# Optimization experiments

Hardware: AMD Instinct MI355X
Metric: run time of the kernel (lower is better)

## Reference

```python
import jax, jax.numpy as jnp
import numpy as np

DIM = 1536
HEADS = 8
DK = 64            # key_size
DV = DIM // HEADS  # value_size = 192
NPF = 32           # num_rel_pos_features
LN_EPS = 1e-3


def central_mask_features(positions, features, seq_len):
    # Borzoi/baskerville central-mask positional basis
    pow_rate = jnp.exp(jnp.log(seq_len + 1.0) / features)
    center_widths = pow_rate ** jnp.arange(1, features + 1, dtype=jnp.float32)
    return (center_widths[None, :] > jnp.abs(positions)[:, None]).astype(jnp.float32)


def get_positional_embed(n, feature_size):
    distances = jnp.arange(-n + 1, n, dtype=jnp.float32)  # (2n-1,)
    emb = central_mask_features(distances, feature_size // 2, n)
    return jnp.concatenate([emb, jnp.sign(distances)[:, None] * emb], axis=-1)  # (2n-1, F)


def relative_shift(x):
    # x: (b, h, n, 2n-1) -> (b, h, n, n), Transformer-XL shift trick
    b, h, t1, t2 = x.shape
    x = jnp.pad(x, ((0, 0), (0, 0), (0, 0), (1, 0)))  # (b,h,n,2n)
    x = x.reshape(b, h, t2 + 1, t1)[:, :, 1:, :]       # (b,h,2n-1,n)
    x = x.reshape(b, h, t1, t2)
    return x[..., :((t2 + 1) // 2)]


def setup_inputs() -> dict:
    key = jax.random.key(0)
    ks = jax.random.split(key, 10)
    s = 0.02
    return {
        "x": jax.random.normal(ks[0], (1, 4096, DIM), jnp.float32),
        "ln_gamma": jnp.ones((DIM,), jnp.float32),
        "ln_beta": jnp.zeros((DIM,), jnp.float32),
        "Wq": jax.random.normal(ks[1], (DIM, HEADS * DK), jnp.float32) * s,
        "Wk": jax.random.normal(ks[2], (DIM, HEADS * DK), jnp.float32) * s,
        "Wv": jax.random.normal(ks[3], (DIM, HEADS * DV), jnp.float32) * s,
        "Wr": jax.random.normal(ks[4], (NPF, HEADS * DK), jnp.float32) * s,
        "Wo": jax.random.normal(ks[5], (HEADS * DV, DIM), jnp.float32) * s,
        "bo": jnp.zeros((DIM,), jnp.float32),
        "rel_content_bias": jax.random.normal(ks[6], (1, HEADS, 1, DK), jnp.float32),
        "rel_pos_bias": jax.random.normal(ks[7], (1, HEADS, 1, DK), jnp.float32),
    }


def reference(x, ln_gamma, ln_beta, Wq, Wk, Wv, Wr, Wo, bo, rel_content_bias, rel_pos_bias):
    B, N, D = x.shape
    # LayerNorm(eps=1e-3)
    mu = jnp.mean(x, axis=-1, keepdims=True)
    var = jnp.mean(jnp.square(x - mu), axis=-1, keepdims=True)
    xn = (x - mu) * jax.lax.rsqrt(var + LN_EPS) * ln_gamma + ln_beta
    # projections -> (B,H,N,d)
    q = (xn @ Wq).reshape(B, N, HEADS, DK).transpose(0, 2, 1, 3) * (DK ** -0.5)
    k = (xn @ Wk).reshape(B, N, HEADS, DK).transpose(0, 2, 1, 3)
    v = (xn @ Wv).reshape(B, N, HEADS, DV).transpose(0, 2, 1, 3)
    content_logits = jnp.einsum('bhid,bhjd->bhij', q + rel_content_bias, k)
    # relative positions (dropout is identity in eval mode)
    pos = get_positional_embed(N, NPF)                       # (2N-1, NPF)
    rel_k = (pos @ Wr).reshape(2 * N - 1, HEADS, DK).transpose(1, 0, 2)  # (H,2N-1,DK)
    rel_logits = jnp.einsum('bhid,hjd->bhij', q + rel_pos_bias, rel_k)   # (B,H,N,2N-1)
    rel_logits = relative_shift(rel_logits)                  # (B,H,N,N)
    attn = jax.nn.softmax(content_logits + rel_logits, axis=-1)
    out = jnp.einsum('bhij,bhjd->bhid', attn, v)
    out = out.transpose(0, 2, 1, 3).reshape(B, N, HEADS * DV)
    return out @ Wo + bo
```

## Files before the change

kernel.cpp:

```cpp
#include <hip/hip_runtime.h>
#include <hip/hip_bf16.h>
#include <math.h>

typedef __hip_bfloat16 bf16;
typedef __attribute__((ext_vector_type(8))) short bf16x8;
typedef __attribute__((ext_vector_type(4))) float f32x4;

#define DIMX 1536
#define NSEQ 4096
#define NHEAD 8
#define DKH 64
#define DVH 192
#define HDK 512
#define HDV 1536
#define KSPLIT 2
#define KVB 32

static __device__ __forceinline__ float b2f(bf16 x){ return __bfloat162float(x); }
static __device__ __forceinline__ bf16 f2b(float x){ return __float2bfloat16(x); }

#define GLD_TO_LDS(gsrc, ldst) __builtin_amdgcn_global_load_lds( \
    (const __attribute__((address_space(1))) unsigned int*)(gsrc), \
    (__attribute__((address_space(3))) unsigned int*)(ldst), 16, 0, 0)

static __device__ __forceinline__ int xcd_swz(int b, int nwg){
  return (b & 7)*(nwg>>3) + (b>>3);
}

__global__ __launch_bounds__(256) void k_cvtT(const float* __restrict__ W, bf16* __restrict__ WT, int K, int N){
  __shared__ float t[32][33];
  int n0 = blockIdx.x<<5, k0 = blockIdx.y<<5;
  int tx = threadIdx.x & 31, ty = threadIdx.x >> 5;
  #pragma unroll
  for (int r=ty; r<32; r+=8) t[r][tx] = W[(size_t)(k0+r)*N + n0 + tx];
  __syncthreads();
  #pragma unroll
  for (int r=ty; r<32; r+=8) WT[(size_t)(n0+r)*K + k0 + tx] = f2b(t[tx][r]);
}

__global__ __launch_bounds__(256) void k_T(const bf16* __restrict__ src, bf16* __restrict__ dst, int R, int C){
  __shared__ bf16 t[64][65];
  int c0 = blockIdx.x<<6, r0 = blockIdx.y<<6;
  int tx = threadIdx.x & 63, ty = threadIdx.x >> 6;
  for (int r=ty; r<64; r+=4) t[r][tx] = src[(size_t)(r0+r)*C + c0 + tx];
  __syncthreads();
  for (int r=ty; r<64; r+=4){
    int dv = c0+r, kv = r0+tx;
    int kvp = (kv & ~31) | ((((kv>>3)&3) ^ ((dv>>1)&3))<<3) | (kv&7);
    dst[(size_t)dv*R + kvp] = t[tx][r];
  }
}

__global__ __launch_bounds__(256) void k_ln(const float* __restrict__ x, const float* __restrict__ g,
                                            const float* __restrict__ b,
                                            bf16* __restrict__ xnh, bf16* __restrict__ xnl){
  int row = blockIdx.x, t = threadIdx.x;
  const float* xr = x + (size_t)row*DIMX;
  float v[6]; float s=0.f, ss=0.f;
  #pragma unroll
  for (int j=0;j<6;++j){ v[j]=xr[t+256*j]; s+=v[j]; ss+=v[j]*v[j]; }
  int lane = t&63, wave = t>>6;
  #pragma unroll
  for (int off=32; off>0; off>>=1){ s += __shfl_down(s,off,64); ss += __shfl_down(ss,off,64); }
  __shared__ float red[8];
  if (lane==0){ red[wave]=s; red[wave+4]=ss; }
  __syncthreads();
  s = red[0]+red[1]+red[2]+red[3];
  ss = red[4]+red[5]+red[6]+red[7];
  float mu = s*(1.f/DIMX);
  float var = ss*(1.f/DIMX) - mu*mu;
  float rstd = rsqrtf(var + 1e-3f);
  #pragma unroll
  for (int j=0;j<6;++j){
    int c = t+256*j;
    float xv = (v[j]-mu)*rstd*g[c] + b[c];
    bf16 hi = f2b(xv);
    xnh[(size_t)row*DIMX + c] = hi;
    xnl[(size_t)row*DIMX + c] = f2b(xv - b2f(hi));
  }
}

template<int EPI>
__global__ __launch_bounds__(256) void k_gemm(const bf16* __restrict__ A, const bf16* __restrict__ BT,
    void* __restrict__ Cout, const float* __restrict__ bias, int M, int N, int K)
{
  __shared__ bf16 As[128][32];
  __shared__ bf16 Bs[128][32];
  int nbx = N>>7;
  int bid = xcd_swz(blockIdx.x, gridDim.x);
  int m0 = (bid / nbx)<<7, n0 = (bid % nbx)<<7;
  int tid = threadIdx.x, wave = tid>>6, lane = tid&63;
  int lr = lane&15, lc = lane>>4;
  int wm = (wave>>1)<<6, wn = (wave&1)<<6;
  f32x4 acc[4][4] = {};
  for (int k0=0; k0<K; k0+=32){
    __syncthreads();
    #pragma unroll
    for (int it=0; it<2; ++it){
      int id = tid + (it<<8);
      int rr = id>>2, cc = id&3;
      unsigned wbase = (unsigned)(((it<<8) + (tid & 192))*16);
      GLD_TO_LDS(A  + (size_t)(m0+rr)*K + k0 + cc*8, (char*)As + wbase);
      GLD_TO_LDS(BT + (size_t)(n0+rr)*K + k0 + cc*8, (char*)Bs + wbase);
    }
    __syncthreads();
    bf16x8 af[4], bfr[4];
    #pragma unroll
    for (int mt=0; mt<4; ++mt) af[mt] = *(const bf16x8*)(&As[wm + mt*16 + lr][lc*8]);
    #pragma unroll
    for (int nt=0; nt<4; ++nt) bfr[nt] = *(const bf16x8*)(&Bs[wn + nt*16 + lr][lc*8]);
    #pragma unroll
    for (int mt=0; mt<4; ++mt)
      #pragma unroll
      for (int nt=0; nt<4; ++nt)
        acc[mt][nt] = __builtin_amdgcn_mfma_f32_16x16x32_bf16(af[mt], bfr[nt], acc[mt][nt], 0,0,0);
  }
  #pragma unroll
  for (int mt=0; mt<4; ++mt){
    #pragma unroll
    for (int nt=0; nt<4; ++nt){
      #pragma unroll
      for (int reg=0; reg<4; ++reg){
        int row = m0 + wm + mt*16 + (lc<<2) + reg;
        int col = n0 + wn + nt*16 + lr;
        if (EPI==0) ((bf16*)Cout)[(size_t)row*N + col] = f2b(acc[mt][nt][reg]);
        else        ((float*)Cout)[(size_t)row*N + col] = acc[mt][nt][reg] + bias[col];
      }
    }
  }
}

template<int EPIQ>
__global__ __launch_bounds__(256) void k_gemm3(const bf16* __restrict__ Ahi, const bf16* __restrict__ Alo,
    const bf16* __restrict__ Bhi,
    bf16* __restrict__ Ohi, bf16* __restrict__ Olo,
    const float* __restrict__ cb, int M, int N, int K)
{
  __shared__ bf16 Ash[128][32];
  __shared__ bf16 Asl[128][32];
  __shared__ bf16 Bsh[128][32];
  int nbx = N>>7;
  int bid = xcd_swz(blockIdx.x, gridDim.x);
  int m0 = (bid / nbx)<<7, n0 = (bid % nbx)<<7;
  int tid = threadIdx.x, wave = tid>>6, lane = tid&63;
  int lr = lane&15, lc = lane>>4;
  int wm = (wave>>1)<<6, wn = (wave&1)<<6;
  f32x4 acc[4][4] = {};
  for (int k0=0; k0<K; k0+=32){
    __syncthreads();
    #pragma unroll
    for (int it=0; it<2; ++it){
      int id = tid + (it<<8);
      int rr = id>>2, cc = id&3;
      unsigned wbase = (unsigned)(((it<<8) + (tid & 192))*16);
      size_t ga = (size_t)(m0+rr)*K + k0 + cc*8;
      size_t gb = (size_t)(n0+rr)*K + k0 + cc*8;
      GLD_TO_LDS(Ahi + ga, (char*)Ash + wbase);
      GLD_TO_LDS(Alo + ga, (char*)Asl + wbase);
      GLD_TO_LDS(Bhi + gb, (char*)Bsh + wbase);
    }
    __syncthreads();
    bf16x8 ah[4], al[4], bh[4];
    #pragma unroll
    for (int mt=0; mt<4; ++mt){
      ah[mt] = *(const bf16x8*)(&Ash[wm + mt*16 + lr][lc*8]);
      al[mt] = *(const bf16x8*)(&Asl[wm + mt*16 + lr][lc*8]);
    }
    #pragma unroll
    for (int nt=0; nt<4; ++nt)
      bh[nt] = *(const bf16x8*)(&Bsh[wn + nt*16 + lr][lc*8]);
    #pragma unroll
    for (int mt=0; mt<4; ++mt)
      #pragma unroll
      for (int nt=0; nt<4; ++nt){
        acc[mt][nt] = __builtin_amdgcn_mfma_f32_16x16x32_bf16(ah[mt], bh[nt], acc[mt][nt], 0,0,0);
        acc[mt][nt] = __builtin_amdgcn_mfma_f32_16x16x32_bf16(al[mt], bh[nt], acc[mt][nt], 0,0,0);
      }
  }
  #pragma unroll
  for (int mt=0; mt<4; ++mt){
    #pragma unroll
    for (int nt=0; nt<4; ++nt){
      #pragma unroll
      for (int reg=0; reg<4; ++reg){
        int row = m0 + wm + mt*16 + (lc<<2) + reg;
        int col = n0 + wn + nt*16 + lr;
        float v = acc[mt][nt][reg];
        int colw = col;
        if (EPIQ==1) v = v*0.125f + cb[col & (HDK-1)];
        else colw = (col & ~63) | ((((col>>3)&7) ^ (row&7))<<3) | (col&7);
        bf16 hi = f2b(v);
        Ohi[(size_t)row*N + colw] = hi;
        Olo[(size_t)row*N + colw] = f2b(v - b2f(hi));
      }
    }
  }
}

__global__ __launch_bounds__(64) void k_abtab(const bf16* __restrict__ qph, const bf16* __restrict__ qpl,
                                              const float* __restrict__ Wr,
                                              const float* __restrict__ cb, const float* __restrict__ pb,
                                              float* __restrict__ ab){
  int i = blockIdx.x, h = blockIdx.y;
  int lane = threadIdx.x;
  __shared__ float qpp[64];
  __shared__ float us[32];
  size_t qi = (size_t)i*HDK + h*DKH + lane;
  int col = h*DKH + lane;
  qpp[lane] = b2f(qph[qi]) + b2f(qpl[qi]) - cb[col] + pb[col];
  __syncthreads();
  if (lane < 32){
    const float* wr = Wr + (size_t)lane*HDK + h*DKH;
    float u=0.f;
    #pragma unroll
    for (int d2=0; d2<64; ++d2) u += wr[d2]*qpp[d2];
    us[lane]=u;
  }
  __syncthreads();
  if (lane < 16){
    float a=0.f, bb=0.f;
    for (int f=15; f>=lane; --f){ a += us[f]; bb += us[16+f]; }
    float* o = ab + ((size_t)h*NSEQ + i)*32;
    o[lane]=a; o[16+lane]=bb;
  }
}

__global__ __launch_bounds__(256,4) void k_attn(
    const bf16* __restrict__ qph, const bf16* __restrict__ qpl,
    const bf16* __restrict__ khs, const bf16* __restrict__ kls,
    const bf16* __restrict__ vts, const float* __restrict__ ab,
    bf16* __restrict__ PO, float2* __restrict__ ML)
{
  int wg = blockIdx.x;
  int h  = wg & 7;
  int qtile = (wg >> 3) & 63;
  int ks = wg >> 9;
  int q0 = qtile * 64;
  int tid = threadIdx.x, wave = tid>>6, lane = tid&63;
  int lr = lane&15, lc = lane>>4;

  __shared__ bf16 Ksh[KVB][64];
  __shared__ bf16 Ksl[KVB][64];
  __shared__ bf16 Vs[DVH][KVB];
  __shared__ bf16 Ps[4][16][36];
  __shared__ float2 ABs[64][17];

  for (int xx=tid; xx<1024; xx+=256){
    int row = xx>>4, g = xx&15;
    const float* src = ab + ((size_t)h*NSEQ + q0 + row)*32;
    ABs[row][g] = make_float2(src[g], src[16+g]);
  }

  bf16x8 qfh[2], qfl[2];
  {
    int row = q0 + wave*16 + lr;
    const bf16* qrh = qph + (size_t)row*HDK + h*DKH;
    const bf16* qrl = qpl + (size_t)row*HDK + h*DKH;
    qfh[0] = *(const bf16x8*)(qrh + 8*lc);
    qfh[1] = *(const bf16x8*)(qrh + 32 + 8*lc);
    qfl[0] = *(const bf16x8*)(qrl + 8*lc);
    qfl[1] = *(const bf16x8*)(qrl + 32 + 8*lc);
  }
  const bf16* Kh = khs + h*DKH;
  const bf16* Kl = kls + h*DKH;
  const bf16* Vt = vts + (size_t)h*DVH*NSEQ;

  f32x4 oacc[12] = {};
  float mrow[4], lrow[4];
  #pragma unroll
  for (int r=0;r<4;++r){ mrow[r]=-3e38f; lrow[r]=0.f; }

  const float RCPL = 1.33329424f;
  int kv_lo = ks * (NSEQ/KSPLIT);
  int kv_hi = kv_lo + NSEQ/KSPLIT;

  for (int kv0=kv_lo; kv0<kv_hi; kv0+=KVB) {
    __syncthreads();
    {
      int r = tid>>3, c = tid&7;
      size_t gk = (size_t)(kv0+r)*HDK + c*8;
      GLD_TO_LDS(Kh + gk, (char*)Ksh + (tid&192)*16);
      GLD_TO_LDS(Kl + gk, (char*)Ksl + (tid&192)*16);
      #pragma unroll
      for (int j=0; j<3; ++j){
        int id = j*256 + tid;
        int vr = id>>2, vc = id&3;
        GLD_TO_LDS(Vt + (size_t)vr*NSEQ + kv0 + vc*8, (char*)Vs + (j*256 + (tid&192))*16);
      }
    }
    __syncthreads();

    f32x4 sf[2];
    #pragma unroll
    for (int ct=0; ct<2; ++ct){
      f32x4 s = {};
      int krow = ct*16 + lr;
      int sw0 = ((lc  ) ^ (krow&7))*8;
      int sw1 = ((lc+4) ^ (krow&7))*8;
      bf16x8 kh0 = *(const bf16x8*)(&Ksh[krow][sw0]);
      bf16x8 kh1 = *(const bf16x8*)(&Ksh[krow][sw1]);
      bf16x8 kl0 = *(const bf16x8*)(&Ksl[krow][sw0]);
      bf16x8 kl1 = *(const bf16x8*)(&Ksl[krow][sw1]);
      s = __builtin_amdgcn_mfma_f32_16x16x32_bf16(qfh[0], kh0, s, 0,0,0);
      s = __builtin_amdgcn_mfma_f32_16x16x32_bf16(qfh[1], kh1, s, 0,0,0);
      s = __builtin_amdgcn_mfma_f32_16x16x32_bf16(qfl[0], kh0, s, 0,0,0);
      s = __builtin_amdgcn_mfma_f32_16x16x32_bf16(qfl[1], kh1, s, 0,0,0);
      s = __builtin_amdgcn_mfma_f32_16x16x32_bf16(qfh[0], kl0, s, 0,0,0);
      s = __builtin_amdgcn_mfma_f32_16x16x32_bf16(qfh[1], kl1, s, 0,0,0);
      sf[ct]=s;
    }
    float mnew[4];
    #pragma unroll
    for (int r=0;r<4;++r) mnew[r]=mrow[r];
    #pragma unroll
    for (int ct=0; ct<2; ++ct){
      int j = kv0 + ct*16 + lr;
      #pragma unroll
      for (int reg=0; reg<4; ++reg){
        int rowloc = wave*16 + 4*lc + reg;
        int dd = j - (q0 + rowloc);
        int ad = dd<0 ? -dd : dd;
        int gg = ad ? (int)(__log2f((float)ad) * RCPL) : 0;
        float2 sb = ABs[rowloc][gg];
        float bias = sb.x + (dd>0 ? sb.y : (dd<0 ? -sb.y : 0.f));
        float sv = sf[ct][reg] + bias;
        sf[ct][reg] = sv;
        mnew[reg] = fmaxf(mnew[reg], sv);
      }
    }
    #pragma unroll
    for (int off=1; off<16; off<<=1){
      #pragma unroll
      for (int r=0;r<4;++r) mnew[r] = fmaxf(mnew[r], __shfl_xor(mnew[r], off, 64));
    }
    bool okl = true;
    #pragma unroll
    for (int r=0;r<4;++r) okl = okl && (mnew[r] - mrow[r] <= 8.f);
    if (!__all(okl)){
      float scl[4];
      #pragma unroll
      for (int r=0;r<4;++r){
        scl[r] = __expf(mrow[r]-mnew[r]);
        mrow[r]=mnew[r];
        lrow[r]*=scl[r];
      }
      #pragma unroll
      for (int t12=0;t12<12;++t12){
        #pragma unroll
        for (int reg=0;reg<4;++reg) oacc[t12][reg]*=scl[reg];
      }
    }
    #pragma unroll
    for (int ct=0; ct<2; ++ct){
      #pragma unroll
      for (int reg=0; reg<4; ++reg){
        float p = __expf(sf[ct][reg]-mrow[reg]);
        lrow[reg]+=p;
        Ps[wave][4*lc+reg][ct*16+lr] = f2b(p);
      }
    }
    bf16x8 pa = *(const bf16x8*)(&Ps[wave][lr][lc*8]);
    #pragma unroll
    for (int t12=0; t12<12; ++t12){
      int vrow = t12*16 + lr;
      bf16x8 v0 = *(const bf16x8*)(&Vs[vrow][(lc ^ ((vrow>>1)&3))*8]);
      oacc[t12] = __builtin_amdgcn_mfma_f32_16x16x32_bf16(pa, v0, oacc[t12], 0,0,0);
    }
  }
  #pragma unroll
  for (int off=1; off<16; off<<=1){
    #pragma unroll
    for (int r=0;r<4;++r) lrow[r] += __shfl_xor(lrow[r], off, 64);
  }
  #pragma unroll
  for (int t12=0;t12<12;++t12){
    #pragma unroll
    for (int reg=0;reg<4;++reg){
      int rowloc = wave*16 + 4*lc + reg;
      PO[((size_t)wg*64 + rowloc)*DVH + t12*16 + lr] = f2b(oacc[t12][reg]);
    }
  }
  if (lr == 0){
    #pragma unroll
    for (int reg=0; reg<4; ++reg){
      int rowloc = wave*16 + 4*lc + reg;
      ML[(size_t)wg*64 + rowloc] = make_float2(mrow[reg], lrow[reg]);
    }
  }
}

__global__ __launch_bounds__(256) void k_comb(const bf16* __restrict__ PO, const float2* __restrict__ ML,
                                              bf16* __restrict__ Obuf){
  int i = blockIdx.x;
  int qtile = i>>6, rl = i&63;
  for (int c=threadIdx.x; c<HDV; c+=256){
    int h = c/DVH, d = c - h*DVH;
    int wg0 = qtile*8 + h, wg1 = 512 + wg0;
    float2 ml0 = ML[(size_t)wg0*64 + rl];
    float2 ml1 = ML[(size_t)wg1*64 + rl];
    float M = fmaxf(ml0.x, ml1.x);
    float w0 = __expf(ml0.x - M), w1 = __expf(ml1.x - M);
    float l = ml0.y*w0 + ml1.y*w1;
    float o = b2f(PO[((size_t)wg0*64 + rl)*DVH + d])*w0
            + b2f(PO[((size_t)wg1*64 + rl)*DVH + d])*w1;
    Obuf[(size_t)i*HDV + c] = f2b(o / l);
  }
}

extern "C" void kernel_launch(void* const* d_in, const int* in_sizes, int n_in,
                              void* d_out, int out_size, void* d_ws, size_t ws_size,
                              hipStream_t stream) {
  const float* x  = (const float*)d_in[0];
  const float* lg = (const float*)d_in[1];
  const float* lb = (const float*)d_in[2];
  const float* Wq = (const float*)d_in[3];
  const float* Wk = (const float*)d_in[4];
  const float* Wv = (const float*)d_in[5];
  const float* Wr = (const float*)d_in[6];
  const float* Wo = (const float*)d_in[7];
  const float* bo = (const float*)d_in[8];
  const float* cb = (const float*)d_in[9];
  const float* pb = (const float*)d_in[10];
  float* out = (float*)d_out;

  char* ws = (char*)d_ws;
  size_t off = 0;
  auto alloc = [&](size_t bytes)->void*{ void* p = ws + off; off += (bytes + 255) & ~(size_t)255; return p; };
  bf16* WoT  = (bf16*)alloc((size_t)DIMX*HDV*2);
  bf16* qph  = (bf16*)alloc((size_t)NSEQ*HDK*2);
  bf16* qpl  = (bf16*)alloc((size_t)NSEQ*HDK*2);
  bf16* kh   = (bf16*)alloc((size_t)NSEQ*HDK*2);
  bf16* kl   = (bf16*)alloc((size_t)NSEQ*HDK*2);
  bf16* vt   = (bf16*)alloc((size_t)HDV*NSEQ*2);
  float* ab  = (float*)alloc((size_t)NHEAD*NSEQ*32*4);
  bf16* Obuf = (bf16*)alloc((size_t)NSEQ*HDV*2);
  float2* ML = (float2*)alloc((size_t)KSPLIT*512*64*sizeof(float2));
  char* scratch = (char*)alloc(0);
  bf16* xnh  = (bf16*)alloc((size_t)NSEQ*DIMX*2);
  bf16* xnl  = (bf16*)alloc((size_t)NSEQ*DIMX*2);
  bf16* v_rm = (bf16*)alloc((size_t)NSEQ*HDV*2);
  bf16* WqT  = (bf16*)alloc((size_t)HDK*DIMX*2);
  bf16* WkT  = (bf16*)alloc((size_t)HDK*DIMX*2);
  bf16* WvT  = (bf16*)alloc((size_t)HDV*DIMX*2);
  bf16* PO   = (bf16*)scratch;
  (void)in_sizes; (void)n_in; (void)out_size; (void)ws_size;

  k_cvtT<<<dim3(HDK/32,  DIMX/32), 256, 0, stream>>>(Wq, WqT, DIMX, HDK);
  k_cvtT<<<dim3(HDK/32,  DIMX/32), 256, 0, stream>>>(Wk, WkT, DIMX, HDK);
  k_cvtT<<<dim3(HDV/32,  DIMX/32), 256, 0, stream>>>(Wv, WvT, DIMX, HDV);
  k_cvtT<<<dim3(DIMX/32, HDV/32),  256, 0, stream>>>(Wo, WoT, HDV, DIMX);
  k_ln<<<NSEQ, 256, 0, stream>>>(x, lg, lb, xnh, xnl);

  k_gemm3<1><<<(NSEQ/128)*(HDK/128), 256, 0, stream>>>(xnh, xnl, WqT, qph, qpl, cb, NSEQ, HDK, DIMX);
  k_gemm3<0><<<(NSEQ/128)*(HDK/128), 256, 0, stream>>>(xnh, xnl, WkT, kh, kl, nullptr, NSEQ, HDK, DIMX);
  k_gemm<0><<<(NSEQ/128)*(HDV/128), 256, 0, stream>>>(xnh, WvT, (void*)v_rm, nullptr, NSEQ, HDV, DIMX);

  k_abtab<<<dim3(NSEQ, NHEAD), 64, 0, stream>>>(qph, qpl, Wr, cb, pb, ab);
  k_T<<<dim3(HDV/64, NSEQ/64), 256, 0, stream>>>(v_rm, vt, NSEQ, HDV);

  k_attn<<<KSPLIT*512, 256, 0, stream>>>(qph, qpl, kh, kl, vt, ab, PO, ML);
  k_comb<<<NSEQ, 256, 0, stream>>>(PO, ML, Obuf);

  k_gemm<1><<<(NSEQ/128)*(DIMX/128), 256, 0, stream>>>(Obuf, WoT, (void*)out, bo, NSEQ, DIMX, HDV);
}
```

Measured before the change: 564.4 us.

## Fuse Q/K projection GEMMs, widen abtab blocks, precompute signed bias table

The Q and K projection GEMMs become one launch over a concatenated transposed weight, with the epilogue choosing Q scaling plus bias or K swizzled storage by column range. The abtab kernel now handles all heads of a row in one 256-thread block with vectorized weight loads. It writes a 34-entry table holding the sign-folded sums a+b, a-b and the zero-distance value. The attention inner loop then does a single table lookup instead of a float2 load plus sign selects. This cuts launches and per-element bias arithmetic, at the cost of a slightly larger table and a more branchy GEMM epilogue.

```diff
diff --git a/kernel.cpp b/kernel.cpp
--- a/kernel.cpp
+++ b/kernel.cpp
@@ -130,16 +130,15 @@
   }
 }
 
-template<int EPIQ>
-__global__ __launch_bounds__(256) void k_gemm3(const bf16* __restrict__ Ahi, const bf16* __restrict__ Alo,
+__global__ __launch_bounds__(256) void k_gemmqk(const bf16* __restrict__ Ahi, const bf16* __restrict__ Alo,
     const bf16* __restrict__ Bhi,
-    bf16* __restrict__ Ohi, bf16* __restrict__ Olo,
-    const float* __restrict__ cb, int M, int N, int K)
+    bf16* __restrict__ qph, bf16* __restrict__ qpl,
+    bf16* __restrict__ kh, bf16* __restrict__ kl, const float* __restrict__ cb)
 {
   __shared__ bf16 Ash[128][32];
   __shared__ bf16 Asl[128][32];
   __shared__ bf16 Bsh[128][32];
-  int nbx = N>>7;
+  const int N = 1024, K = DIMX, nbx = 8;
   int bid = xcd_swz(blockIdx.x, gridDim.x);
   int m0 = (bid / nbx)<<7, n0 = (bid % nbx)<<7;
   int tid = threadIdx.x, wave = tid>>6, lane = tid&63;
@@ -177,6 +176,7 @@
         acc[mt][nt] = __builtin_amdgcn_mfma_f32_16x16x32_bf16(al[mt], bh[nt], acc[mt][nt], 0,0,0);
       }
   }
+  bool isQ = (n0 < 512);
   #pragma unroll
   for (int mt=0; mt<4; ++mt){
     #pragma unroll
@@ -186,42 +186,58 @@
         int row = m0 + wm + mt*16 + (lc<<2) + reg;
         int col = n0 + wn + nt*16 + lr;
         float v = acc[mt][nt][reg];
-        int colw = col;
-        if (EPIQ==1) v = v*0.125f + cb[col & (HDK-1)];
-        else colw = (col & ~63) | ((((col>>3)&7) ^ (row&7))<<3) | (col&7);
-        bf16 hi = f2b(v);
-        Ohi[(size_t)row*N + colw] = hi;
-        Olo[(size_t)row*N + colw] = f2b(v - b2f(hi));
-      }
-    }
-  }
-}
-
-__global__ __launch_bounds__(64) void k_abtab(const bf16* __restrict__ qph, const bf16* __restrict__ qpl,
-                                              const float* __restrict__ Wr,
-                                              const float* __restrict__ cb, const float* __restrict__ pb,
-                                              float* __restrict__ ab){
-  int i = blockIdx.x, h = blockIdx.y;
-  int lane = threadIdx.x;
-  __shared__ float qpp[64];
-  __shared__ float us[32];
-  size_t qi = (size_t)i*HDK + h*DKH + lane;
-  int col = h*DKH + lane;
-  qpp[lane] = b2f(qph[qi]) + b2f(qpl[qi]) - cb[col] + pb[col];
+        if (isQ){
+          v = v*0.125f + cb[col];
+          bf16 hi = f2b(v);
+          qph[(size_t)row*HDK + col] = hi;
+          qpl[(size_t)row*HDK + col] = f2b(v - b2f(hi));
+        } else {
+          int ck = col - 512;
+          int colw = (ck & ~63) | ((((ck>>3)&7) ^ (row&7))<<3) | (ck&7);
+          bf16 hi = f2b(v);
+          kh[(size_t)row*HDK + colw] = hi;
+          kl[(size_t)row*HDK + colw] = f2b(v - b2f(hi));
+        }
+      }
+    }
+  }
+}
+
+__global__ __launch_bounds__(256) void k_abtab(const bf16* __restrict__ qph, const bf16* __restrict__ qpl,
+                                               const float* __restrict__ Wr,
+                                               const float* __restrict__ cb, const float* __restrict__ pb,
+                                               float* __restrict__ ab){
+  int i = blockIdx.x, t = threadIdx.x;
+  __shared__ float qpp[HDK];
+  __shared__ float us[NHEAD][32];
+  #pragma unroll
+  for (int j=0;j<2;++j){
+    int c = t + j*256;
+    size_t qi = (size_t)i*HDK + c;
+    qpp[c] = b2f(qph[qi]) + b2f(qpl[qi]) - cb[c] + pb[c];
+  }
   __syncthreads();
-  if (lane < 32){
-    const float* wr = Wr + (size_t)lane*HDK + h*DKH;
-    float u=0.f;
-    #pragma unroll
-    for (int d2=0; d2<64; ++d2) u += wr[d2]*qpp[d2];
-    us[lane]=u;
+  {
+    int h = t>>5, f = t&31;
+    const float* wr = Wr + (size_t)f*HDK + h*DKH;
+    const float* qh = qpp + h*DKH;
+    float u = 0.f;
+    #pragma unroll
+    for (int d=0; d<64; d+=4){
+      float4 w4 = *(const float4*)(wr + d);
+      u += w4.x*qh[d] + w4.y*qh[d+1] + w4.z*qh[d+2] + w4.w*qh[d+3];
+    }
+    us[h][f] = u;
   }
   __syncthreads();
-  if (lane < 16){
+  if (t < 128){
+    int h2 = t>>4, f2 = t&15;
     float a=0.f, bb=0.f;
-    for (int f=15; f>=lane; --f){ a += us[f]; bb += us[16+f]; }
-    float* o = ab + ((size_t)h*NSEQ + i)*32;
-    o[lane]=a; o[16+lane]=bb;
+    for (int g=15; g>=f2; --g){ a += us[h2][g]; bb += us[h2][16+g]; }
+    float* o = ab + ((size_t)h2*NSEQ + i)*34;
+    o[f2] = a + bb;
+    o[17+f2] = a - bb;
+    if (f2 == 0){ o[16] = a; o[33] = a; }
   }
 }
 
@@ -243,12 +259,11 @@
   __shared__ bf16 Ksl[KVB][64];
   __shared__ bf16 Vs[DVH][KVB];
   __shared__ bf16 Ps[4][16][36];
-  __shared__ float2 ABs[64][17];
-
-  for (int xx=tid; xx<1024; xx+=256){
-    int row = xx>>4, g = xx&15;
-    const float* src = ab + ((size_t)h*NSEQ + q0 + row)*32;
-    ABs[row][g] = make_float2(src[g], src[16+g]);
+  __shared__ float Ts[64][34];
+
+  {
+    const float* src = ab + ((size_t)h*NSEQ + q0)*34;
+    for (int xx=tid; xx<64*34; xx+=256) ((float*)Ts)[xx] = src[xx];
   }
 
   bf16x8 qfh[2], qfl[2];
@@ -320,9 +335,8 @@
         int rowloc = wave*16 + 4*lc + reg;
         int dd = j - (q0 + rowloc);
         int ad = dd<0 ? -dd : dd;
-        int gg = ad ? (int)(__log2f((float)ad) * RCPL) : 0;
-        float2 sb = ABs[rowloc][gg];
-        float bias = sb.x + (dd>0 ? sb.y : (dd<0 ? -sb.y : 0.f));
+        int gg = ad ? (int)(__log2f((float)ad) * RCPL) : 16;
+        float bias = Ts[rowloc][(dd<0 ? 17:0) + gg];
         float sv = sf[ct][reg] + bias;
         sf[ct][reg] = sv;
         mnew[reg] = fmaxf(mnew[reg], sv);
@@ -432,30 +446,28 @@
   bf16* kh   = (bf16*)alloc((size_t)NSEQ*HDK*2);
   bf16* kl   = (bf16*)alloc((size_t)NSEQ*HDK*2);
   bf16* vt   = (bf16*)alloc((size_t)HDV*NSEQ*2);
-  float* ab  = (float*)alloc((size_t)NHEAD*NSEQ*32*4);
+  float* ab  = (float*)alloc((size_t)NHEAD*NSEQ*34*4);
   bf16* Obuf = (bf16*)alloc((size_t)NSEQ*HDV*2);
   float2* ML = (float2*)alloc((size_t)KSPLIT*512*64*sizeof(float2));
   char* scratch = (char*)alloc(0);
   bf16* xnh  = (bf16*)alloc((size_t)NSEQ*DIMX*2);
   bf16* xnl  = (bf16*)alloc((size_t)NSEQ*DIMX*2);
   bf16* v_rm = (bf16*)alloc((size_t)NSEQ*HDV*2);
-  bf16* WqT  = (bf16*)alloc((size_t)HDK*DIMX*2);
-  bf16* WkT  = (bf16*)alloc((size_t)HDK*DIMX*2);
+  bf16* WqkT = (bf16*)alloc((size_t)1024*DIMX*2);
   bf16* WvT  = (bf16*)alloc((size_t)HDV*DIMX*2);
   bf16* PO   = (bf16*)scratch;
   (void)in_sizes; (void)n_in; (void)out_size; (void)ws_size;
 
-  k_cvtT<<<dim3(HDK/32,  DIMX/32), 256, 0, stream>>>(Wq, WqT, DIMX, HDK);
-  k_cvtT<<<dim3(HDK/32,  DIMX/32), 256, 0, stream>>>(Wk, WkT, DIMX, HDK);
+  k_cvtT<<<dim3(HDK/32,  DIMX/32), 256, 0, stream>>>(Wq, WqkT, DIMX, HDK);
+  k_cvtT<<<dim3(HDK/32,  DIMX/32), 256, 0, stream>>>(Wk, WqkT + (size_t)512*DIMX, DIMX, HDK);
   k_cvtT<<<dim3(HDV/32,  DIMX/32), 256, 0, stream>>>(Wv, WvT, DIMX, HDV);
   k_cvtT<<<dim3(DIMX/32, HDV/32),  256, 0, stream>>>(Wo, WoT, HDV, DIMX);
   k_ln<<<NSEQ, 256, 0, stream>>>(x, lg, lb, xnh, xnl);
 
-  k_gemm3<1><<<(NSEQ/128)*(HDK/128), 256, 0, stream>>>(xnh, xnl, WqT, qph, qpl, cb, NSEQ, HDK, DIMX);
-  k_gemm3<0><<<(NSEQ/128)*(HDK/128), 256, 0, stream>>>(xnh, xnl, WkT, kh, kl, nullptr, NSEQ, HDK, DIMX);
+  k_gemmqk<<<(NSEQ/128)*(1024/128), 256, 0, stream>>>(xnh, xnl, WqkT, qph, qpl, kh, kl, cb);
   k_gemm<0><<<(NSEQ/128)*(HDV/128), 256, 0, stream>>>(xnh, WvT, (void*)v_rm, nullptr, NSEQ, HDV, DIMX);
 
-  k_abtab<<<dim3(NSEQ, NHEAD), 64, 0, stream>>>(qph, qpl, Wr, cb, pb, ab);
+  k_abtab<<<NSEQ, 256, 0, stream>>>(qph, qpl, Wr, cb, pb, ab);
   k_T<<<dim3(HDV/64, NSEQ/64), 256, 0, stream>>>(v_rm, vt, NSEQ, HDV);
 
   k_attn<<<KSPLIT*512, 256, 0, stream>>>(qph, qpl, kh, kl, vt, ab, PO, ML);
```

Result: faster. 511.5 us (-9.4%).
